# Optimization experiments

Hardware: AMD Instinct MI355X
Metric: run time of the kernel (lower is better)

## Reference

```python
import math
import jax, jax.numpy as jnp
import numpy as np

B, Q, K, D = 32, 1024, 1024, 128
MASK_VALUE = -1000000.0


def setup_inputs() -> dict:
    key = jax.random.key(0)
    kq, kk, kv, kl = jax.random.split(key, 4)
    return {
        "queries": jax.random.normal(kq, (B, Q, D), dtype=jnp.float32),
        "keys": jax.random.normal(kk, (B, K, D), dtype=jnp.float32),
        "values": jax.random.normal(kv, (B, K, D), dtype=jnp.float32),
        "valid_lens": jax.random.randint(kl, (B,), 1, K + 1, dtype=jnp.int32),
    }


def reference(queries, keys, values, valid_lens):
    d = queries.shape[-1]
    # scores: [B, Q, K]
    scores = jnp.einsum("bqd,bkd->bqk", queries, keys) / math.sqrt(d)
    # key-padding mask: position k valid iff k < valid_lens[b] (broadcast over queries)
    mask = jnp.arange(keys.shape[1])[None, None, :] < valid_lens[:, None, None]
    scores = jnp.where(mask, scores, MASK_VALUE)
    attn = jax.nn.softmax(scores, axis=-1)
    # dropout p=0.0 -> identity
    return jnp.einsum("bqk,bkv->bqv", attn, values)
```

## Files before the change

### kernel.cpp

```cpp
#include <hip/hip_runtime.h>
#include <math.h>

typedef _Float16 f16;
typedef __attribute__((ext_vector_type(8))) _Float16 f16x8;
typedef __attribute__((ext_vector_type(4))) _Float16 f16x4;
typedef __attribute__((ext_vector_type(4))) float f32x4;

constexpr int BATCH = 32;
constexpr int QL = 1024;
constexpr int KL = 1024;
constexpr int D = 128;
constexpr int BQ = 64;
constexpr int BK = 64;
constexpr int DKP = 136;
constexpr int BKP = 72;

#define CSC 0.12752863187087177f

static __device__ __forceinline__ f16x4 pk4(float x, float y, float z, float w) {
  auto a = __builtin_amdgcn_cvt_pkrtz(x, y);
  auto b = __builtin_amdgcn_cvt_pkrtz(z, w);
  f16x4 h;
  h[0] = (f16)a[0]; h[1] = (f16)a[1]; h[2] = (f16)b[0]; h[3] = (f16)b[1];
  return h;
}
static __device__ __forceinline__ f16x8 pk8(float4 u, float4 v) {
  f16x4 a = pk4(u.x, u.y, u.z, u.w);
  f16x4 b = pk4(v.x, v.y, v.z, v.w);
  f16x8 h;
  h[0] = a[0]; h[1] = a[1]; h[2] = a[2]; h[3] = a[3];
  h[4] = b[0]; h[5] = b[1]; h[6] = b[2]; h[7] = b[3];
  return h;
}

template <int CTRL>
static __device__ __forceinline__ float dppf(float v) {
  int x = __float_as_int(v);
  x = __builtin_amdgcn_update_dpp(x, x, CTRL, 0xf, 0xf, false);
  return __int_as_float(x);
}
static __device__ __forceinline__ float rmax16(float v) {
  v = fmaxf(v, dppf<0xB1>(v));
  v = fmaxf(v, dppf<0x4E>(v));
  v = fmaxf(v, dppf<0x141>(v));
  v = fmaxf(v, dppf<0x140>(v));
  return v;
}
static __device__ __forceinline__ float rsum16(float v) {
  v += dppf<0xB1>(v);
  v += dppf<0x4E>(v);
  v += dppf<0x141>(v);
  v += dppf<0x140>(v);
  return v;
}

__global__ __launch_bounds__(256, 2)
void attn_fwd(const float* __restrict__ Qp, const float* __restrict__ Kp,
              const float* __restrict__ Vp, const int* __restrict__ VLp,
              float* __restrict__ Op) {
  __shared__ f16 sK[2][BK][DKP];
  __shared__ f16 sVT[2][D][BKP];
  __shared__ f16 sP[4][16][BKP];
  __shared__ int sN[32];
  __shared__ int sB;

  const int tid  = threadIdx.x;
  const int wave = tid >> 6, lane = tid & 63;
  const int l16  = lane & 15, quad = lane >> 4;

  if (tid < 32) sN[tid] = (VLp[tid] + BK - 1) / BK;
  __syncthreads();
  if (tid < 32) {
    int nb = sN[tid], r = 0;
    #pragma unroll
    for (int k = 0; k < 32; ++k) {
      int nk = sN[k];
      r += (nk > nb) || (nk == nb && k < tid);
    }
    sN[tid] = r;
  }
  __syncthreads();
  const int c = blockIdx.x & 255;
  const int s = (blockIdx.x < 256) ? c : (511 - c);
  if (tid < 32 && sN[tid] == (s >> 4)) sB = tid;
  __syncthreads();
  const int b  = sB;
  const int qt = s & 15;
  const int vl = VLp[b];

  const float* Kb = Kp + (size_t)b * KL * D;
  const float* Vb = Vp + (size_t)b * KL * D;
  const int ntiles = (vl + BK - 1) / BK;

  float4 kreg[8], vreg[8];

  {
    const float4* Kt = (const float4*)Kb;
    #pragma unroll
    for (int i = 0; i < 4; ++i) {
      int cc = tid + i * 256;
      int row = cc >> 4, d04 = (cc & 15) * 2;
      kreg[2 * i]     = Kt[row * 32 + d04];
      kreg[2 * i + 1] = Kt[row * 32 + d04 + 1];
    }
    #pragma unroll
    for (int i = 0; i < 2; ++i) {
      int f = tid + i * 256;
      const float* base = Vb + (size_t)((f & 15) * 4) * D + (f >> 4) * 4;
      vreg[i * 4 + 0] = *(const float4*)(base);
      vreg[i * 4 + 1] = *(const float4*)(base + D);
      vreg[i * 4 + 2] = *(const float4*)(base + 2 * D);
      vreg[i * 4 + 3] = *(const float4*)(base + 3 * D);
    }
  }

  const float* Qb = Qp + ((size_t)(b * QL + qt * BQ + wave * 16 + l16)) * D;
  f16x8 qfrag[4];
  #pragma unroll
  for (int kc = 0; kc < 4; ++kc) {
    const float* p = Qb + kc * 32 + quad * 8;
    qfrag[kc] = pk8(*(const float4*)p, *(const float4*)(p + 4));
  }

  float m2[4]   = {-INFINITY, -INFINITY, -INFINITY, -INFINITY};
  float lsum[4] = {0.f, 0.f, 0.f, 0.f};
  f32x4 o[8];
  #pragma unroll
  for (int dt = 0; dt < 8; ++dt) o[dt] = (f32x4){0.f, 0.f, 0.f, 0.f};

  #pragma unroll
  for (int i = 0; i < 4; ++i) {
    int cc = tid + i * 256;
    int row = cc >> 4, d0 = (cc & 15) * 8;
    int rp = (row & 3) * 16 + (row >> 2);
    *(f16x8*)&sK[0][rp][d0] = pk8(kreg[2 * i], kreg[2 * i + 1]);
  }
  #pragma unroll
  for (int i = 0; i < 2; ++i) {
    int f = tid + i * 256;
    int k0 = (f & 15) * 4, d0 = (f >> 4) * 4;
    float4 r0 = vreg[i*4+0], r1 = vreg[i*4+1], r2 = vreg[i*4+2], r3 = vreg[i*4+3];
    *(f16x4*)&sVT[0][d0 + 0][k0] = pk4(r0.x, r1.x, r2.x, r3.x);
    *(f16x4*)&sVT[0][d0 + 1][k0] = pk4(r0.y, r1.y, r2.y, r3.y);
    *(f16x4*)&sVT[0][d0 + 2][k0] = pk4(r0.z, r1.z, r2.z, r3.z);
    *(f16x4*)&sVT[0][d0 + 3][k0] = pk4(r0.w, r1.w, r2.w, r3.w);
  }
  __syncthreads();

  for (int t = 0; t < ntiles; ++t) {
    const int cur = t & 1, nxt = cur ^ 1;
    const bool more = (t + 1 < ntiles);

    if (more) {
      const float4* Kt = (const float4*)(Kb + (size_t)(t + 1) * BK * D);
      #pragma unroll
      for (int i = 0; i < 4; ++i) {
        int cc = tid + i * 256;
        int row = cc >> 4, d04 = (cc & 15) * 2;
        kreg[2 * i]     = Kt[row * 32 + d04];
        kreg[2 * i + 1] = Kt[row * 32 + d04 + 1];
      }
      const float* Vt = Vb + (size_t)(t + 1) * BK * D;
      #pragma unroll
      for (int i = 0; i < 2; ++i) {
        int f = tid + i * 256;
        const float* base = Vt + (size_t)((f & 15) * 4) * D + (f >> 4) * 4;
        vreg[i * 4 + 0] = *(const float4*)(base);
        vreg[i * 4 + 1] = *(const float4*)(base + D);
        vreg[i * 4 + 2] = *(const float4*)(base + 2 * D);
        vreg[i * 4 + 3] = *(const float4*)(base + 3 * D);
      }
    }

    f32x4 sv[4];
    #pragma unroll
    for (int ct = 0; ct < 4; ++ct) {
      f32x4 cacc = (f32x4){0.f, 0.f, 0.f, 0.f};
      #pragma unroll
      for (int kc = 0; kc < 4; ++kc) {
        f16x8 kf = *(const f16x8*)&sK[cur][ct * 16 + l16][kc * 32 + quad * 8];
        cacc = __builtin_amdgcn_mfma_f32_16x16x32_f16(qfrag[kc], kf, cacc, 0, 0, 0);
      }
      sv[ct] = cacc;
    }

    #pragma unroll
    for (int ct = 0; ct < 4; ++ct) {
      bool ok = (t * BK + l16 * 4 + ct) < vl;
      #pragma unroll
      for (int r = 0; r < 4; ++r)
        sv[ct][r] = ok ? sv[ct][r] * CSC : -1.0e9f;
    }

    float mnew[4], alpha[4];
    #pragma unroll
    for (int r = 0; r < 4; ++r) {
      float v = fmaxf(fmaxf(sv[0][r], sv[1][r]), fmaxf(sv[2][r], sv[3][r]));
      v = rmax16(v);
      mnew[r]  = fmaxf(m2[r], v);
      alpha[r] = __builtin_amdgcn_exp2f(m2[r] - mnew[r]);
      m2[r]    = mnew[r];
    }
    #pragma unroll
    for (int r = 0; r < 4; ++r) {
      float ls = 0.f;
      #pragma unroll
      for (int ct = 0; ct < 4; ++ct) {
        float p = __builtin_amdgcn_exp2f(sv[ct][r] - mnew[r]);
        sv[ct][r] = p;
        ls += p;
      }
      lsum[r] = lsum[r] * alpha[r] + rsum16(ls);
      *(f16x4*)&sP[wave][quad * 4 + r][l16 * 4] =
          pk4(sv[0][r], sv[1][r], sv[2][r], sv[3][r]);
      #pragma unroll
      for (int dt = 0; dt < 8; ++dt) o[dt][r] *= alpha[r];
    }

    asm volatile("s_waitcnt lgkmcnt(0)" ::: "memory");

    #pragma unroll
    for (int ks = 0; ks < 2; ++ks) {
      f16x8 pf = *(const f16x8*)&sP[wave][l16][ks * 32 + quad * 8];
      #pragma unroll
      for (int dt = 0; dt < 8; ++dt) {
        f16x8 vf = *(const f16x8*)&sVT[cur][dt * 16 + l16][ks * 32 + quad * 8];
        o[dt] = __builtin_amdgcn_mfma_f32_16x16x32_f16(pf, vf, o[dt], 0, 0, 0);
      }
    }

    if (more) {
      #pragma unroll
      for (int i = 0; i < 4; ++i) {
        int cc = tid + i * 256;
        int row = cc >> 4, d0 = (cc & 15) * 8;
        int rp = (row & 3) * 16 + (row >> 2);
        *(f16x8*)&sK[nxt][rp][d0] = pk8(kreg[2 * i], kreg[2 * i + 1]);
      }
      #pragma unroll
      for (int i = 0; i < 2; ++i) {
        int f = tid + i * 256;
        int k0 = (f & 15) * 4, d0 = (f >> 4) * 4;
        float4 r0 = vreg[i*4+0], r1 = vreg[i*4+1], r2 = vreg[i*4+2], r3 = vreg[i*4+3];
        *(f16x4*)&sVT[nxt][d0 + 0][k0] = pk4(r0.x, r1.x, r2.x, r3.x);
        *(f16x4*)&sVT[nxt][d0 + 1][k0] = pk4(r0.y, r1.y, r2.y, r3.y);
        *(f16x4*)&sVT[nxt][d0 + 2][k0] = pk4(r0.z, r1.z, r2.z, r3.z);
        *(f16x4*)&sVT[nxt][d0 + 3][k0] = pk4(r0.w, r1.w, r2.w, r3.w);
      }
    }
    __syncthreads();
  }

  float* Ob = Op + ((size_t)(b * QL + qt * BQ + wave * 16)) * D;
  #pragma unroll
  for (int r = 0; r < 4; ++r) {
    float inv = 1.0f / lsum[r];
    int row = quad * 4 + r;
    #pragma unroll
    for (int dt = 0; dt < 8; ++dt)
      Ob[(size_t)row * D + dt * 16 + l16] = o[dt][r] * inv;
  }
}

extern "C" void kernel_launch(void* const* d_in, const int* in_sizes, int n_in,
                              void* d_out, int out_size, void* d_ws, size_t ws_size,
                              hipStream_t stream) {
  const float* Qp = (const float*)d_in[0];
  const float* Kp = (const float*)d_in[1];
  const float* Vp = (const float*)d_in[2];
  const int*   VL = (const int*)d_in[3];
  float* Op = (float*)d_out;

  attn_fwd<<<dim3(QL / BQ * BATCH), dim3(256), 0, stream>>>(Qp, Kp, Vp, VL, Op);
}
```

Baseline: 118.3 us.

## Software-pipeline QK^T one tile ahead and prefetch K/V two tiles ahead

Restructures the main loop so the QK^T MFMAs for tile t+1 run while tile t's softmax and PV matmul are processed, and global loads for tile t+2 are issued early. The aim is to overlap softmax latency and global memory latency with matrix work. The cost is an extra __syncthreads per iteration, more live registers (svn), and possibly lower occupancy under launch_bounds(256,2).

```diff
diff --git a/kernel.cpp b/kernel.cpp
--- a/kernel.cpp
+++ b/kernel.cpp
@@ -94,8 +94,8 @@
 
   float4 kreg[8], vreg[8];
 
-  {
-    const float4* Kt = (const float4*)Kb;
+  auto issue_loads = [&](int t) {
+    const float4* Kt = (const float4*)(Kb + (size_t)t * BK * D);
     #pragma unroll
     for (int i = 0; i < 4; ++i) {
       int cc = tid + i * 256;
@@ -103,16 +103,36 @@
       kreg[2 * i]     = Kt[row * 32 + d04];
       kreg[2 * i + 1] = Kt[row * 32 + d04 + 1];
     }
+    const float* Vt = Vb + (size_t)t * BK * D;
     #pragma unroll
     for (int i = 0; i < 2; ++i) {
       int f = tid + i * 256;
-      const float* base = Vb + (size_t)((f & 15) * 4) * D + (f >> 4) * 4;
+      const float* base = Vt + (size_t)((f & 15) * 4) * D + (f >> 4) * 4;
       vreg[i * 4 + 0] = *(const float4*)(base);
       vreg[i * 4 + 1] = *(const float4*)(base + D);
       vreg[i * 4 + 2] = *(const float4*)(base + 2 * D);
       vreg[i * 4 + 3] = *(const float4*)(base + 3 * D);
     }
-  }
+  };
+  auto drain = [&](int buf) {
+    #pragma unroll
+    for (int i = 0; i < 4; ++i) {
+      int cc = tid + i * 256;
+      int row = cc >> 4, d0 = (cc & 15) * 8;
+      int rp = (row & 3) * 16 + (row >> 2);
+      *(f16x8*)&sK[buf][rp][d0] = pk8(kreg[2 * i], kreg[2 * i + 1]);
+    }
+    #pragma unroll
+    for (int i = 0; i < 2; ++i) {
+      int f = tid + i * 256;
+      int k0 = (f & 15) * 4, d0 = (f >> 4) * 4;
+      float4 r0 = vreg[i*4+0], r1 = vreg[i*4+1], r2 = vreg[i*4+2], r3 = vreg[i*4+3];
+      *(f16x4*)&sVT[buf][d0 + 0][k0] = pk4(r0.x, r1.x, r2.x, r3.x);
+      *(f16x4*)&sVT[buf][d0 + 1][k0] = pk4(r0.y, r1.y, r2.y, r3.y);
+      *(f16x4*)&sVT[buf][d0 + 2][k0] = pk4(r0.z, r1.z, r2.z, r3.z);
+      *(f16x4*)&sVT[buf][d0 + 3][k0] = pk4(r0.w, r1.w, r2.w, r3.w);
+    }
+  };
 
   const float* Qb = Qp + ((size_t)(b * QL + qt * BQ + wave * 16 + l16)) * D;
   f16x8 qfrag[4];
@@ -122,67 +142,40 @@
     qfrag[kc] = pk8(*(const float4*)p, *(const float4*)(p + 4));
   }
 
+  auto s_mfma = [&](int buf, f32x4* out) {
+    #pragma unroll
+    for (int ct = 0; ct < 4; ++ct) {
+      f32x4 cacc = (f32x4){0.f, 0.f, 0.f, 0.f};
+      #pragma unroll
+      for (int kc = 0; kc < 4; ++kc) {
+        f16x8 kf = *(const f16x8*)&sK[buf][ct * 16 + l16][kc * 32 + quad * 8];
+        cacc = __builtin_amdgcn_mfma_f32_16x16x32_f16(qfrag[kc], kf, cacc, 0, 0, 0);
+      }
+      out[ct] = cacc;
+    }
+  };
+
   float m2[4]   = {-INFINITY, -INFINITY, -INFINITY, -INFINITY};
   float lsum[4] = {0.f, 0.f, 0.f, 0.f};
   f32x4 o[8];
   #pragma unroll
   for (int dt = 0; dt < 8; ++dt) o[dt] = (f32x4){0.f, 0.f, 0.f, 0.f};
 
-  #pragma unroll
-  for (int i = 0; i < 4; ++i) {
-    int cc = tid + i * 256;
-    int row = cc >> 4, d0 = (cc & 15) * 8;
-    int rp = (row & 3) * 16 + (row >> 2);
-    *(f16x8*)&sK[0][rp][d0] = pk8(kreg[2 * i], kreg[2 * i + 1]);
-  }
-  #pragma unroll
-  for (int i = 0; i < 2; ++i) {
-    int f = tid + i * 256;
-    int k0 = (f & 15) * 4, d0 = (f >> 4) * 4;
-    float4 r0 = vreg[i*4+0], r1 = vreg[i*4+1], r2 = vreg[i*4+2], r3 = vreg[i*4+3];
-    *(f16x4*)&sVT[0][d0 + 0][k0] = pk4(r0.x, r1.x, r2.x, r3.x);
-    *(f16x4*)&sVT[0][d0 + 1][k0] = pk4(r0.y, r1.y, r2.y, r3.y);
-    *(f16x4*)&sVT[0][d0 + 2][k0] = pk4(r0.z, r1.z, r2.z, r3.z);
-    *(f16x4*)&sVT[0][d0 + 3][k0] = pk4(r0.w, r1.w, r2.w, r3.w);
-  }
+  f32x4 sv[4], svn[4];
+
+  issue_loads(0);
+  drain(0);
+  if (ntiles > 1) issue_loads(1);
+  __syncthreads();
+  s_mfma(0, sv);
+  if (ntiles > 1) drain(1);
   __syncthreads();
 
   for (int t = 0; t < ntiles; ++t) {
     const int cur = t & 1, nxt = cur ^ 1;
-    const bool more = (t + 1 < ntiles);
-
-    if (more) {
-      const float4* Kt = (const float4*)(Kb + (size_t)(t + 1) * BK * D);
-      #pragma unroll
-      for (int i = 0; i < 4; ++i) {
-        int cc = tid + i * 256;
-        int row = cc >> 4, d04 = (cc & 15) * 2;
-        kreg[2 * i]     = Kt[row * 32 + d04];
-        kreg[2 * i + 1] = Kt[row * 32 + d04 + 1];
-      }
-      const float* Vt = Vb + (size_t)(t + 1) * BK * D;
-      #pragma unroll
-      for (int i = 0; i < 2; ++i) {
-        int f = tid + i * 256;
-        const float* base = Vt + (size_t)((f & 15) * 4) * D + (f >> 4) * 4;
-        vreg[i * 4 + 0] = *(const float4*)(base);
-        vreg[i * 4 + 1] = *(const float4*)(base + D);
-        vreg[i * 4 + 2] = *(const float4*)(base + 2 * D);
-        vreg[i * 4 + 3] = *(const float4*)(base + 3 * D);
-      }
-    }
-
-    f32x4 sv[4];
-    #pragma unroll
-    for (int ct = 0; ct < 4; ++ct) {
-      f32x4 cacc = (f32x4){0.f, 0.f, 0.f, 0.f};
-      #pragma unroll
-      for (int kc = 0; kc < 4; ++kc) {
-        f16x8 kf = *(const f16x8*)&sK[cur][ct * 16 + l16][kc * 32 + quad * 8];
-        cacc = __builtin_amdgcn_mfma_f32_16x16x32_f16(qfrag[kc], kf, cacc, 0, 0, 0);
-      }
-      sv[ct] = cacc;
-    }
+
+    if (t + 1 < ntiles) s_mfma(nxt, svn);
+    if (t + 2 < ntiles) issue_loads(t + 2);
 
     #pragma unroll
     for (int ct = 0; ct < 4; ++ct) {
@@ -191,7 +184,6 @@
       for (int r = 0; r < 4; ++r)
         sv[ct][r] = ok ? sv[ct][r] * CSC : -1.0e9f;
     }
-
     float mnew[4], alpha[4];
     #pragma unroll
     for (int r = 0; r < 4; ++r) {
@@ -229,26 +221,12 @@
       }
     }
 
-    if (more) {
-      #pragma unroll
-      for (int i = 0; i < 4; ++i) {
-        int cc = tid + i * 256;
-        int row = cc >> 4, d0 = (cc & 15) * 8;
-        int rp = (row & 3) * 16 + (row >> 2);
-        *(f16x8*)&sK[nxt][rp][d0] = pk8(kreg[2 * i], kreg[2 * i + 1]);
-      }
-      #pragma unroll
-      for (int i = 0; i < 2; ++i) {
-        int f = tid + i * 256;
-        int k0 = (f & 15) * 4, d0 = (f >> 4) * 4;
-        float4 r0 = vreg[i*4+0], r1 = vreg[i*4+1], r2 = vreg[i*4+2], r3 = vreg[i*4+3];
-        *(f16x4*)&sVT[nxt][d0 + 0][k0] = pk4(r0.x, r1.x, r2.x, r3.x);
-        *(f16x4*)&sVT[nxt][d0 + 1][k0] = pk4(r0.y, r1.y, r2.y, r3.y);
-        *(f16x4*)&sVT[nxt][d0 + 2][k0] = pk4(r0.z, r1.z, r2.z, r3.z);
-        *(f16x4*)&sVT[nxt][d0 + 3][k0] = pk4(r0.w, r1.w, r2.w, r3.w);
-      }
-    }
     __syncthreads();
+    if (t + 2 < ntiles) drain(cur);
+    __syncthreads();
+
+    #pragma unroll
+    for (int ct = 0; ct < 4; ++ct) sv[ct] = svn[ct];
   }
 
   float* Ob = Op + ((size_t)(b * QL + qt * BQ + wave * 16)) * D;
```

Measured after the change: 121.5 us. 1.03x slower.
